# Kernel tuning notes

Measured on AMD Instinct MI355X. Metric: run time of the kernel, lower is better.

## Reference

```python
import jax, jax.numpy as jnp
import numpy as np

CLIP = 5.0  # clip_value from init


def setup_inputs() -> dict:
    key = jax.random.key(0)
    ks = jax.random.split(key, 6)
    B, T, I, H = 128, 1024, 256, 512
    s = 1.0 / np.sqrt(H)
    return {
        "x": jax.random.normal(ks[0], (B, T, I), dtype=jnp.float32),
        "h0": jax.random.normal(ks[1], (1, H), dtype=jnp.float32),
        "w_ih": jax.random.normal(ks[2], (3 * H, I), dtype=jnp.float32) * s,
        "w_hh": jax.random.normal(ks[3], (3 * H, H), dtype=jnp.float32) * s,
        "b_ih": jax.random.normal(ks[4], (3 * H,), dtype=jnp.float32) * s,
        "b_hh": jax.random.normal(ks[5], (3 * H,), dtype=jnp.float32) * s,
    }


def reference(x, h0, w_ih, w_hh, b_ih, b_hh):
    # x: [B, T, I], h0: [1, H]
    B = x.shape[0]
    h_init = jnp.tile(h0, (B, 1))  # [B, H]
    # Precompute all input projections in one big GEMM: [T, B, 3H]
    gi_all = jnp.einsum('bti,gi->tbg', x, w_ih) + b_ih

    def step(h, gi):
        gh = h @ w_hh.T + b_hh                      # [B, 3H]
        ir, iz, inn = jnp.split(gi, 3, axis=-1)
        hr, hz, hn = jnp.split(gh, 3, axis=-1)
        r = jax.nn.sigmoid(ir + hr)
        z = jax.nn.sigmoid(iz + hz)
        n = jnp.tanh(inn + r * hn)
        h_new = (1.0 - z) * n + z * h
        h_new = jnp.clip(h_new, -CLIP, CLIP)
        return h_new, h_new

    h_last, out = jax.lax.scan(step, h_init, gi_all)  # out: [T, B, H]
    output = jnp.transpose(out, (1, 0, 2))            # [B, T, H]
    return output, h_last
```

## Files before the change

### kernel.cpp

```cpp
#include <hip/hip_runtime.h>
#include <math.h>

#define T_SEQ 1024
#define B_SZ  128
#define I_SZ  256
#define H_SZ  512
#define G_SZ  1536

#define NBS   8
#define MB    16
#define NHS   16
#define HB    32
#define GB    96
#define NTHR  384
#define PGB   384

#define SENT32 0x7FFF7FFFu

typedef _Float16 f16;
typedef _Float16 half8 __attribute__((ext_vector_type(8)));
typedef _Float16 f16x4 __attribute__((ext_vector_type(4)));
typedef float f32x4 __attribute__((ext_vector_type(4)));
typedef unsigned uint32x4 __attribute__((ext_vector_type(4)));

__device__ __forceinline__ f32x4 cload_f4(const void* p) {
    f32x4 v;
    asm volatile("global_load_dwordx4 %0, %1, off sc0 sc1" : "=v"(v) : "v"(p));
    return v;
}
__device__ __forceinline__ void cstore_f4(void* p, f32x4 v) {
    asm volatile("global_store_dwordx4 %0, %1, off sc0 sc1" :: "v"(p), "v"(v) : "memory");
}
__device__ __forceinline__ void cstore_u32(void* p, unsigned v) {
    asm volatile("global_store_dword %0, %1, off sc0 sc1" :: "v"(p), "v"(v) : "memory");
}
__device__ __forceinline__ f16x4 load_f16x4_nw(const void* p) {
    f16x4 v;
    asm volatile("global_load_dwordx2 %0, %1, off" : "=v"(v) : "v"(p));
    return v;
}
__device__ __forceinline__ void wait_vm0() {
    asm volatile("s_waitcnt vmcnt(0)" ::: "memory");
    __builtin_amdgcn_sched_barrier(0);
}
__device__ __forceinline__ bool stale4(f32x4 v) {
    uint32x4 u = __builtin_bit_cast(uint32x4, v);
    return (u[0] == SENT32) | (u[1] == SENT32) | (u[2] == SENT32) | (u[3] == SENT32);
}

__global__ void setup_kernel(const float* __restrict__ w_ih,
                             const float* __restrict__ w_hh,
                             const float* __restrict__ h0,
                             f16* __restrict__ wp16,
                             f16* __restrict__ wf16,
                             f16* __restrict__ hbuf) {
    const int i0 = blockIdx.x * blockDim.x + threadIdx.x;
    const int stride = gridDim.x * blockDim.x;
    for (int i = i0; i < I_SZ * G_SZ; i += stride)
        wp16[i] = (f16)w_ih[i];
    for (int i = i0; i < NHS * GB * H_SZ; i += stride) {
        int hs  = i / (GB * H_SZ);
        int rem = i % (GB * H_SZ);
        int gl = rem / H_SZ, k = rem % H_SZ;
        int gate = gl >> 5, c = gl & 31;
        int gg = gate * H_SZ + hs * HB + c;
        wf16[i] = (f16)w_hh[(size_t)gg * H_SZ + k];
    }
    const int hph = B_SZ * H_SZ;
    const f16 sent = __builtin_bit_cast(f16, (unsigned short)0x7FFF);
    for (int i = i0; i < 3 * hph; i += stride) {
        if (i < hph) hbuf[i] = (f16)h0[i & (H_SZ - 1)];
        else         hbuf[i] = sent;
    }
}

__global__ __launch_bounds__(512, 1)
void proj_kernel(const float* __restrict__ x,
                 const f16* __restrict__ wp16,
                 const float* __restrict__ b_ih,
                 f16* __restrict__ gi16) {
    const int t  = blockIdx.x >> 2;
    const int g0 = (blockIdx.x & 3) * PGB;
    const int tid  = threadIdx.x;
    const int wid  = tid >> 6;
    const int lane = tid & 63;
    const int col  = lane & 15;
    const int krow = lane >> 4;

    __shared__ __align__(16) unsigned char x_lds[128 * 512];

    #pragma unroll
    for (int j = 0; j < 8; ++j) {
        int idx = tid + j * 512;
        int b = idx >> 5, k16 = idx & 31;
        const float* xp = x + ((size_t)b * T_SEQ + t) * I_SZ + k16 * 8;
        float4 v0 = *reinterpret_cast<const float4*>(xp);
        float4 v1 = *reinterpret_cast<const float4*>(xp + 4);
        half8 hv;
        hv[0] = (f16)v0.x; hv[1] = (f16)v0.y; hv[2] = (f16)v0.z; hv[3] = (f16)v0.w;
        hv[4] = (f16)v1.x; hv[5] = (f16)v1.y; hv[6] = (f16)v1.z; hv[7] = (f16)v1.w;
        unsigned addr = ((unsigned)(b * 512 + k16 * 16)) ^ (((unsigned)(b & 7)) << 4);
        *reinterpret_cast<half8*>(x_lds + addr) = hv;
    }

    const int gw0 = g0 + wid * 48;
    half8 af[3][8];
    #pragma unroll
    for (int m = 0; m < 3; ++m)
        #pragma unroll
        for (int k = 0; k < 8; ++k)
            af[m][k] = *reinterpret_cast<const half8*>(
                wp16 + (size_t)(gw0 + m * 16 + col) * I_SZ + k * 32 + krow * 8);

    float bias[3][4];
    #pragma unroll
    for (int m = 0; m < 3; ++m)
        #pragma unroll
        for (int r = 0; r < 4; ++r)
            bias[m][r] = b_ih[gw0 + m * 16 + krow * 4 + r];

    __syncthreads();

    #pragma unroll
    for (int nt = 0; nt < 8; ++nt) {
        const int b0 = nt * 16;
        f32x4 acc0 = {0.f,0.f,0.f,0.f}, acc1 = {0.f,0.f,0.f,0.f}, acc2 = {0.f,0.f,0.f,0.f};
        const int brow = b0 + col;
        const unsigned bswz = ((unsigned)(brow & 7)) << 4;
        #pragma unroll
        for (int k = 0; k < 8; ++k) {
            half8 bf = *reinterpret_cast<const half8*>(
                x_lds + (((unsigned)(brow * 512 + k * 64 + krow * 16)) ^ bswz));
            acc0 = __builtin_amdgcn_mfma_f32_16x16x32_f16(af[0][k], bf, acc0, 0, 0, 0);
            acc1 = __builtin_amdgcn_mfma_f32_16x16x32_f16(af[1][k], bf, acc1, 0, 0, 0);
            acc2 = __builtin_amdgcn_mfma_f32_16x16x32_f16(af[2][k], bf, acc2, 0, 0, 0);
        }
        const int pbs = brow >> 4;
        const int pm  = brow & 15;
        #pragma unroll
        for (int r = 0; r < 4; ++r) {
            int gr = gw0 + krow * 4 + r;
            gi16[((size_t)(t * NBS + pbs) * G_SZ + gr)      * MB + pm] = (f16)(acc0[r] + bias[0][r]);
            gi16[((size_t)(t * NBS + pbs) * G_SZ + gr + 16) * MB + pm] = (f16)(acc1[r] + bias[1][r]);
            gi16[((size_t)(t * NBS + pbs) * G_SZ + gr + 32) * MB + pm] = (f16)(acc2[r] + bias[2][r]);
        }
    }
}

__global__ __launch_bounds__(NTHR, 1)
void gru_persist(const f16* __restrict__ gi,
                 const f16* __restrict__ wf16,
                 const float* __restrict__ h0,
                 const float* __restrict__ b_hh,
                 f16* __restrict__ hbuf,
                 float* __restrict__ out) {
    const int bs  = blockIdx.x & (NBS - 1);
    const int hs  = blockIdx.x >> 3;
    const int tid = threadIdx.x;

    __shared__ __align__(16) unsigned char h_lds[MB * H_SZ * 2];
    __shared__ float act_r[MB][HB + 1];
    __shared__ float act_z[MB][HB + 1];
    __shared__ float act_n[MB][HB + 1];
    __shared__ float act_i[MB][HB + 1];

    const int wid  = tid >> 6;
    const int lane = tid & 63;
    const int gate = wid >> 1;
    const int sub  = wid & 1;
    const int col  = lane & 15;
    const int krow = lane >> 4;
    const int c_local = sub * 16 + col;
    const int g_glob  = gate * H_SZ + hs * HB + c_local;

    half8 bfrag[16];
    {
        const f16* wp = wf16 + ((size_t)hs * GB + gate * HB + c_local) * H_SZ
                             + krow * 8;
        #pragma unroll
        for (int kk = 0; kk < 16; ++kk)
            bfrag[kk] = *reinterpret_cast<const half8*>(wp + kk * 32);
    }
    const float bias = b_hh[g_glob];

    const int cb = tid >> 4;
    const int cc = (tid & 15) * 2;
    float hm0 = 0.f, hm1 = 0.f;
    if (tid < 256) { hm0 = h0[hs * HB + cc]; hm1 = h0[hs * HB + cc + 1]; }

    const unsigned a_base = (unsigned)(col * 1024 + krow * 16);
    const unsigned a_swz  = ((unsigned)(col & 7)) << 4;

    const int i0 = tid, i1 = tid + NTHR, i2 = tid + 2 * NTHR;
    const bool has2 = (i2 < 1024);
    const f32x4 sentv = __builtin_bit_cast(f32x4,
        (uint32x4){SENT32, SENT32, SENT32, SENT32});

    const size_t phase_sz = (size_t)B_SZ * H_SZ;

    for (int t = 0; t < T_SEQ; ++t) {
        const int pc = t % 3;
        const int pn = (t + 1) % 3;
        const int pa = (t + 2) % 3;
        const f16* hin = hbuf + (size_t)pc * phase_sz;
        f16* hnx = hbuf + (size_t)pn * phase_sz;
        f16* harm = hbuf + (size_t)pa * phase_sz;

        f16x4 gv = load_f16x4_nw(
            gi + ((size_t)(t * NBS + bs) * G_SZ + g_glob) * MB + krow * 4);

        const f16* a0p = hin + (size_t)(bs * MB + (i0 >> 6)) * H_SZ + (i0 & 63) * 8;
        const f16* a1p = hin + (size_t)(bs * MB + (i1 >> 6)) * H_SZ + (i1 & 63) * 8;
        const f16* a2p = hin + (size_t)(bs * MB + (i2 >> 6)) * H_SZ + (i2 & 63) * 8;
        f32x4 v0 = cload_f4(a0p);
        f32x4 v1 = cload_f4(a1p);
        f32x4 v2;
        if (has2) v2 = cload_f4(a2p);
        wait_vm0();
        {
            int guard = 0;
            bool s0 = stale4(v0), s1 = stale4(v1), s2 = has2 && stale4(v2);
            while (__any(s0 | s1 | s2)) {
                if (s0) v0 = cload_f4((const void*)a0p);
                if (s1) v1 = cload_f4((const void*)a1p);
                if (s2) v2 = cload_f4((const void*)a2p);
                wait_vm0();
                s0 = stale4(v0); s1 = stale4(v1); s2 = has2 && stale4(v2);
                if (++guard > (1 << 20)) break;
            }
        }

        {
            unsigned l0 = ((unsigned)((i0 >> 6) * 1024 + (i0 & 63) * 16))
                          ^ (((unsigned)((i0 >> 6) & 7)) << 4);
            *reinterpret_cast<f32x4*>(h_lds + l0) = v0;
            unsigned l1 = ((unsigned)((i1 >> 6) * 1024 + (i1 & 63) * 16))
                          ^ (((unsigned)((i1 >> 6) & 7)) << 4);
            *reinterpret_cast<f32x4*>(h_lds + l1) = v1;
            if (has2) {
                unsigned l2 = ((unsigned)((i2 >> 6) * 1024 + (i2 & 63) * 16))
                              ^ (((unsigned)((i2 >> 6) & 7)) << 4);
                *reinterpret_cast<f32x4*>(h_lds + l2) = v2;
            }
            if (tid < 64) {
                int row = tid >> 2, g = tid & 3;
                cstore_f4(harm + (size_t)(bs * MB + row) * H_SZ + hs * HB + g * 8,
                          sentv);
            }
        }
        __syncthreads();

        f32x4 acc = {0.f, 0.f, 0.f, 0.f};
        #pragma unroll
        for (int kk = 0; kk < 16; ++kk) {
            half8 av = *reinterpret_cast<const half8*>(
                h_lds + ((a_base + kk * 64) ^ a_swz));
            acc = __builtin_amdgcn_mfma_f32_16x16x32_f16(av, bfrag[kk], acc, 0, 0, 0);
        }
        wait_vm0();

        if (gate == 0) {
            #pragma unroll
            for (int r = 0; r < 4; ++r)
                act_r[krow * 4 + r][c_local] =
                    1.f / (1.f + __expf(-(acc[r] + bias + (float)gv[r])));
        } else if (gate == 1) {
            #pragma unroll
            for (int r = 0; r < 4; ++r)
                act_z[krow * 4 + r][c_local] =
                    1.f / (1.f + __expf(-(acc[r] + bias + (float)gv[r])));
        } else {
            #pragma unroll
            for (int r = 0; r < 4; ++r) {
                act_n[krow * 4 + r][c_local] = acc[r] + bias;
                act_i[krow * 4 + r][c_local] = (float)gv[r];
            }
        }
        __syncthreads();

        if (tid < 256) {
            float r0 = act_r[cb][cc],     r1 = act_r[cb][cc + 1];
            float z0 = act_z[cb][cc],     z1 = act_z[cb][cc + 1];
            float a0 = act_i[cb][cc]     + r0 * act_n[cb][cc];
            float a1 = act_i[cb][cc + 1] + r1 * act_n[cb][cc + 1];
            float n0 = 1.f - 2.f / (__expf(2.f * a0) + 1.f);
            float n1 = 1.f - 2.f / (__expf(2.f * a1) + 1.f);
            float hn0 = (1.f - z0) * n0 + z0 * hm0;
            float hn1 = (1.f - z1) * n1 + z1 * hm1;
            hn0 = fminf(fmaxf(hn0, -5.f), 5.f);
            hn1 = fminf(fmaxf(hn1, -5.f), 5.f);
            hm0 = hn0; hm1 = hn1;

            const int bg = bs * MB + cb;
            const int hg = hs * HB + cc;

            f16 p0 = (f16)hn0, p1 = (f16)hn1;
            unsigned pack = (unsigned)__builtin_bit_cast(unsigned short, p0)
                          | ((unsigned)__builtin_bit_cast(unsigned short, p1) << 16);
            cstore_u32(hnx + (size_t)bg * H_SZ + hg, pack);

            *reinterpret_cast<float2*>(
                out + ((size_t)bg * T_SEQ + t) * H_SZ + hg) = make_float2(hn0, hn1);

            if (t == T_SEQ - 1)
                *reinterpret_cast<float2*>(
                    out + (size_t)B_SZ * T_SEQ * H_SZ + (size_t)bg * H_SZ + hg) =
                    make_float2(hn0, hn1);
        }
    }
}

extern "C" void kernel_launch(void* const* d_in, const int* in_sizes, int n_in,
                              void* d_out, int out_size, void* d_ws, size_t ws_size,
                              hipStream_t stream) {
    const float* x    = (const float*)d_in[0];
    const float* h0   = (const float*)d_in[1];
    const float* w_ih = (const float*)d_in[2];
    const float* w_hh = (const float*)d_in[3];
    const float* b_ih = (const float*)d_in[4];
    const float* b_hh = (const float*)d_in[5];
    float* out = (float*)d_out;

    char* p = (char*)d_ws;
    f16* wp16 = (f16*)p;   p += (size_t)I_SZ * G_SZ * 2;
    f16* wf16 = (f16*)p;   p += (size_t)NHS * GB * H_SZ * 2;
    f16* hbuf = (f16*)p;   p += (size_t)3 * B_SZ * H_SZ * 2;
    f16* gi   = (f16*)p;

    setup_kernel<<<512, 256, 0, stream>>>(w_ih, w_hh, h0, wp16, wf16, hbuf);

    proj_kernel<<<T_SEQ * 4, 512, 0, stream>>>(x, wp16, b_ih, gi);

    gru_persist<<<NBS * NHS, NTHR, 0, stream>>>(gi, wf16, h0, b_hh, hbuf, out);
}
```

Measured before the change: 3.353 ms.

## Halve persistent GRU grid; each block handles two batch slices with 64-wide hidden tiles

The persistent recurrent kernel now runs 32 blocks instead of 128. Each block owns 64 hidden columns (192 gate rows) and serially processes two batch slices per timestep. Half the recurrent weights stay in registers and the other half live in LDS. The h-state buffers become per-batch-slice triple buffers, and the update step writes 4 elements per thread. The intent is to cut the number of blocks in the cross-block spin-wait handshake and the global h traffic per step. The cost is twice the MFMA and LDS work per block, two serialized chains per step, and a heavier LDS footprint.

Measured after the change: 4.899 ms. 1.46x slower.

```diff
diff --git a/kernel.cpp b/kernel.cpp
--- a/kernel.cpp
+++ b/kernel.cpp
@@ -8,12 +8,15 @@
 #define G_SZ  1536
 
 #define NBS   8
+#define NPC   4
 #define MB    16
-#define NHS   16
-#define HB    32
-#define GB    96
+#define NHS   8
+#define HB    64
+#define GB    192
 #define NTHR  384
 #define PGB   384
+#define PH    (MB * H_SZ)
+#define SLC   (3 * PH)
 
 #define SENT32 0x7FFF7FFFu
 
@@ -21,6 +24,7 @@
 typedef _Float16 half8 __attribute__((ext_vector_type(8)));
 typedef _Float16 f16x4 __attribute__((ext_vector_type(4)));
 typedef float f32x4 __attribute__((ext_vector_type(4)));
+typedef unsigned uint32x2 __attribute__((ext_vector_type(2)));
 typedef unsigned uint32x4 __attribute__((ext_vector_type(4)));
 
 __device__ __forceinline__ f32x4 cload_f4(const void* p) {
@@ -31,8 +35,8 @@
 __device__ __forceinline__ void cstore_f4(void* p, f32x4 v) {
     asm volatile("global_store_dwordx4 %0, %1, off sc0 sc1" :: "v"(p), "v"(v) : "memory");
 }
-__device__ __forceinline__ void cstore_u32(void* p, unsigned v) {
-    asm volatile("global_store_dword %0, %1, off sc0 sc1" :: "v"(p), "v"(v) : "memory");
+__device__ __forceinline__ void cstore_u2(void* p, uint32x2 v) {
+    asm volatile("global_store_dwordx2 %0, %1, off sc0 sc1" :: "v"(p), "v"(v) : "memory");
 }
 __device__ __forceinline__ f16x4 load_f16x4_nw(const void* p) {
     f16x4 v;
@@ -62,15 +66,16 @@
         int hs  = i / (GB * H_SZ);
         int rem = i % (GB * H_SZ);
         int gl = rem / H_SZ, k = rem % H_SZ;
-        int gate = gl >> 5, c = gl & 31;
+        int gate = gl >> 6, c = gl & 63;
         int gg = gate * H_SZ + hs * HB + c;
         wf16[i] = (f16)w_hh[(size_t)gg * H_SZ + k];
     }
-    const int hph = B_SZ * H_SZ;
+    const int htot = NBS * SLC;
     const f16 sent = __builtin_bit_cast(f16, (unsigned short)0x7FFF);
-    for (int i = i0; i < 3 * hph; i += stride) {
-        if (i < hph) hbuf[i] = (f16)h0[i & (H_SZ - 1)];
-        else         hbuf[i] = sent;
+    for (int i = i0; i < htot; i += stride) {
+        int j = i % SLC;
+        int phase = j / PH;
+        hbuf[i] = (phase == 0) ? (f16)h0[j & (H_SZ - 1)] : sent;
     }
 }
 
@@ -154,10 +159,13 @@
                  const float* __restrict__ b_hh,
                  f16* __restrict__ hbuf,
                  float* __restrict__ out) {
-    const int bs  = blockIdx.x & (NBS - 1);
-    const int hs  = blockIdx.x >> 3;
-    const int tid = threadIdx.x;
-
+    const int pcid = blockIdx.x & (NPC - 1);
+    const int hs   = blockIdx.x >> 2;
+    const int bsA  = pcid * 2;
+    const int bsB  = pcid * 2 + 1;
+    const int tid  = threadIdx.x;
+
+    __shared__ __align__(16) unsigned char w_lds[96 * 1024];
     __shared__ __align__(16) unsigned char h_lds[MB * H_SZ * 2];
     __shared__ float act_r[MB][HB + 1];
     __shared__ float act_z[MB][HB + 1];
@@ -166,147 +174,179 @@
 
     const int wid  = tid >> 6;
     const int lane = tid & 63;
-    const int gate = wid >> 1;
-    const int sub  = wid & 1;
     const int col  = lane & 15;
     const int krow = lane >> 4;
-    const int c_local = sub * 16 + col;
-    const int g_glob  = gate * H_SZ + hs * HB + c_local;
-
+
+    const int ttR = wid, ttL = wid + 6;
+    const int gateR = ttR >> 2, gateL = ttL >> 2;
+    const int gcR = (ttR & 3) * 16 + col;
+    const int gcL = (ttL & 3) * 16 + col;
+    const int ggR = gateR * H_SZ + hs * HB + gcR;
+    const int ggL = gateL * H_SZ + hs * HB + gcL;
+    const float biasR = b_hh[ggR];
+    const float biasL = b_hh[ggL];
+
+    const f16* wbase = wf16 + (size_t)hs * GB * H_SZ;
+
+    for (int i = tid; i < 96 * 64; i += NTHR) {
+        int r = i >> 6, k8 = i & 63;
+        f32x4 v = *reinterpret_cast<const f32x4*>(
+            wbase + (size_t)(96 + r) * H_SZ + k8 * 8);
+        unsigned addr = ((unsigned)(r * 1024 + k8 * 16)) ^ (((unsigned)(r & 7)) << 4);
+        *reinterpret_cast<f32x4*>(w_lds + addr) = v;
+    }
     half8 bfrag[16];
     {
-        const f16* wp = wf16 + ((size_t)hs * GB + gate * HB + c_local) * H_SZ
-                             + krow * 8;
+        const f16* wp = wbase + (size_t)(ttR * 16 + col) * H_SZ + krow * 8;
         #pragma unroll
         for (int kk = 0; kk < 16; ++kk)
             bfrag[kk] = *reinterpret_cast<const half8*>(wp + kk * 32);
     }
-    const float bias = b_hh[g_glob];
-
-    const int cb = tid >> 4;
-    const int cc = (tid & 15) * 2;
-    float hm0 = 0.f, hm1 = 0.f;
-    if (tid < 256) { hm0 = h0[hs * HB + cc]; hm1 = h0[hs * HB + cc + 1]; }
+
+    const int cb  = tid >> 4;
+    const int cc4 = (tid & 15) * 4;
+    f32x4 hmA = {0.f,0.f,0.f,0.f}, hmB = {0.f,0.f,0.f,0.f};
+    if (tid < 256) {
+        #pragma unroll
+        for (int u = 0; u < 4; ++u) { hmA[u] = h0[hs * HB + cc4 + u]; hmB[u] = hmA[u]; }
+    }
 
     const unsigned a_base = (unsigned)(col * 1024 + krow * 16);
     const unsigned a_swz  = ((unsigned)(col & 7)) << 4;
+    const unsigned b_base = (unsigned)((wid * 16 + col) * 1024 + krow * 16);
 
     const int i0 = tid, i1 = tid + NTHR, i2 = tid + 2 * NTHR;
-    const bool has2 = (i2 < 1024);
+    const bool has2 = (tid < 256);
     const f32x4 sentv = __builtin_bit_cast(f32x4,
         (uint32x4){SENT32, SENT32, SENT32, SENT32});
 
-    const size_t phase_sz = (size_t)B_SZ * H_SZ;
+    f16* hbA = hbuf + (size_t)bsA * SLC;
+    f16* hbB = hbuf + (size_t)bsB * SLC;
+
+    __syncthreads();
 
     for (int t = 0; t < T_SEQ; ++t) {
-        const int pc = t % 3;
-        const int pn = (t + 1) % 3;
-        const int pa = (t + 2) % 3;
-        const f16* hin = hbuf + (size_t)pc * phase_sz;
-        f16* hnx = hbuf + (size_t)pn * phase_sz;
-        f16* harm = hbuf + (size_t)pa * phase_sz;
-
-        f16x4 gv = load_f16x4_nw(
-            gi + ((size_t)(t * NBS + bs) * G_SZ + g_glob) * MB + krow * 4);
-
-        const f16* a0p = hin + (size_t)(bs * MB + (i0 >> 6)) * H_SZ + (i0 & 63) * 8;
-        const f16* a1p = hin + (size_t)(bs * MB + (i1 >> 6)) * H_SZ + (i1 & 63) * 8;
-        const f16* a2p = hin + (size_t)(bs * MB + (i2 >> 6)) * H_SZ + (i2 & 63) * 8;
-        f32x4 v0 = cload_f4(a0p);
-        f32x4 v1 = cload_f4(a1p);
-        f32x4 v2;
-        if (has2) v2 = cload_f4(a2p);
-        wait_vm0();
-        {
-            int guard = 0;
-            bool s0 = stale4(v0), s1 = stale4(v1), s2 = has2 && stale4(v2);
-            while (__any(s0 | s1 | s2)) {
-                if (s0) v0 = cload_f4((const void*)a0p);
-                if (s1) v1 = cload_f4((const void*)a1p);
-                if (s2) v2 = cload_f4((const void*)a2p);
-                wait_vm0();
-                s0 = stale4(v0); s1 = stale4(v1); s2 = has2 && stale4(v2);
-                if (++guard > (1 << 20)) break;
-            }
-        }
-
-        {
-            unsigned l0 = ((unsigned)((i0 >> 6) * 1024 + (i0 & 63) * 16))
-                          ^ (((unsigned)((i0 >> 6) & 7)) << 4);
-            *reinterpret_cast<f32x4*>(h_lds + l0) = v0;
-            unsigned l1 = ((unsigned)((i1 >> 6) * 1024 + (i1 & 63) * 16))
-                          ^ (((unsigned)((i1 >> 6) & 7)) << 4);
-            *reinterpret_cast<f32x4*>(h_lds + l1) = v1;
-            if (has2) {
-                unsigned l2 = ((unsigned)((i2 >> 6) * 1024 + (i2 & 63) * 16))
-                              ^ (((unsigned)((i2 >> 6) & 7)) << 4);
-                *reinterpret_cast<f32x4*>(h_lds + l2) = v2;
-            }
-            if (tid < 64) {
-                int row = tid >> 2, g = tid & 3;
-                cstore_f4(harm + (size_t)(bs * MB + row) * H_SZ + hs * HB + g * 8,
-                          sentv);
-            }
-        }
-        __syncthreads();
-
-        f32x4 acc = {0.f, 0.f, 0.f, 0.f};
-        #pragma unroll
-        for (int kk = 0; kk < 16; ++kk) {
-            half8 av = *reinterpret_cast<const half8*>(
-                h_lds + ((a_base + kk * 64) ^ a_swz));
-            acc = __builtin_amdgcn_mfma_f32_16x16x32_f16(av, bfrag[kk], acc, 0, 0, 0);
-        }
-        wait_vm0();
-
-        if (gate == 0) {
+        const size_t pcO = (size_t)(t % 3) * PH;
+        const size_t pnO = (size_t)((t + 1) % 3) * PH;
+        const size_t paO = (size_t)((t + 2) % 3) * PH;
+
+        auto chain = [&](f16* hb, int bs, f32x4& hm) {
+            f16x4 gvR = load_f16x4_nw(
+                gi + ((size_t)(t * NBS + bs) * G_SZ + ggR) * MB + krow * 4);
+            f16x4 gvL = load_f16x4_nw(
+                gi + ((size_t)(t * NBS + bs) * G_SZ + ggL) * MB + krow * 4);
+
+            const f16* hin = hb + pcO;
+            const f16* a0p = hin + (i0 >> 6) * H_SZ + (i0 & 63) * 8;
+            const f16* a1p = hin + (i1 >> 6) * H_SZ + (i1 & 63) * 8;
+            const f16* a2p = hin + (i2 >> 6) * H_SZ + (i2 & 63) * 8;
+            f32x4 v0 = cload_f4(a0p);
+            f32x4 v1 = cload_f4(a1p);
+            f32x4 v2;
+            if (has2) v2 = cload_f4(a2p);
+            wait_vm0();
+            {
+                int guard = 0;
+                bool s0 = stale4(v0), s1 = stale4(v1), s2 = has2 && stale4(v2);
+                while (__any(s0 | s1 | s2)) {
+                    if (s0) v0 = cload_f4((const void*)a0p);
+                    if (s1) v1 = cload_f4((const void*)a1p);
+                    if (s2) v2 = cload_f4((const void*)a2p);
+                    wait_vm0();
+                    s0 = stale4(v0); s1 = stale4(v1); s2 = has2 && stale4(v2);
+                    if (++guard > (1 << 20)) break;
+                }
+            }
+
+            {
+                unsigned l0 = ((unsigned)((i0 >> 6) * 1024 + (i0 & 63) * 16))
+                              ^ (((unsigned)((i0 >> 6) & 7)) << 4);
+                *reinterpret_cast<f32x4*>(h_lds + l0) = v0;
+                unsigned l1 = ((unsigned)((i1 >> 6) * 1024 + (i1 & 63) * 16))
+                              ^ (((unsigned)((i1 >> 6) & 7)) << 4);
+                *reinterpret_cast<f32x4*>(h_lds + l1) = v1;
+                if (has2) {
+                    unsigned l2 = ((unsigned)((i2 >> 6) * 1024 + (i2 & 63) * 16))
+                                  ^ (((unsigned)((i2 >> 6) & 7)) << 4);
+                    *reinterpret_cast<f32x4*>(h_lds + l2) = v2;
+                }
+                if (tid < 128) {
+                    int row = tid >> 3, g = tid & 7;
+                    cstore_f4(hb + paO + (size_t)row * H_SZ + hs * HB + g * 8,
+                              sentv);
+                }
+            }
+            __syncthreads();
+
+            f32x4 accR = {0.f,0.f,0.f,0.f}, accL = {0.f,0.f,0.f,0.f};
             #pragma unroll
-            for (int r = 0; r < 4; ++r)
-                act_r[krow * 4 + r][c_local] =
-                    1.f / (1.f + __expf(-(acc[r] + bias + (float)gv[r])));
-        } else if (gate == 1) {
-            #pragma unroll
-            for (int r = 0; r < 4; ++r)
-                act_z[krow * 4 + r][c_local] =
-                    1.f / (1.f + __expf(-(acc[r] + bias + (float)gv[r])));
-        } else {
-            #pragma unroll
-            for (int r = 0; r < 4; ++r) {
-                act_n[krow * 4 + r][c_local] = acc[r] + bias;
-                act_i[krow * 4 + r][c_local] = (float)gv[r];
-            }
-        }
-        __syncthreads();
-
-        if (tid < 256) {
-            float r0 = act_r[cb][cc],     r1 = act_r[cb][cc + 1];
-            float z0 = act_z[cb][cc],     z1 = act_z[cb][cc + 1];
-            float a0 = act_i[cb][cc]     + r0 * act_n[cb][cc];
-            float a1 = act_i[cb][cc + 1] + r1 * act_n[cb][cc + 1];
-            float n0 = 1.f - 2.f / (__expf(2.f * a0) + 1.f);
-            float n1 = 1.f - 2.f / (__expf(2.f * a1) + 1.f);
-            float hn0 = (1.f - z0) * n0 + z0 * hm0;
-            float hn1 = (1.f - z1) * n1 + z1 * hm1;
-            hn0 = fminf(fmaxf(hn0, -5.f), 5.f);
-            hn1 = fminf(fmaxf(hn1, -5.f), 5.f);
-            hm0 = hn0; hm1 = hn1;
-
-            const int bg = bs * MB + cb;
-            const int hg = hs * HB + cc;
-
-            f16 p0 = (f16)hn0, p1 = (f16)hn1;
-            unsigned pack = (unsigned)__builtin_bit_cast(unsigned short, p0)
-                          | ((unsigned)__builtin_bit_cast(unsigned short, p1) << 16);
-            cstore_u32(hnx + (size_t)bg * H_SZ + hg, pack);
-
-            *reinterpret_cast<float2*>(
-                out + ((size_t)bg * T_SEQ + t) * H_SZ + hg) = make_float2(hn0, hn1);
-
-            if (t == T_SEQ - 1)
-                *reinterpret_cast<float2*>(
-                    out + (size_t)B_SZ * T_SEQ * H_SZ + (size_t)bg * H_SZ + hg) =
-                    make_float2(hn0, hn1);
-        }
+            for (int kk = 0; kk < 16; ++kk) {
+                half8 av = *reinterpret_cast<const half8*>(
+                    h_lds + ((a_base + kk * 64) ^ a_swz));
+                half8 bv = *reinterpret_cast<const half8*>(
+                    w_lds + ((b_base + kk * 64) ^ a_swz));
+                accR = __builtin_amdgcn_mfma_f32_16x16x32_f16(av, bfrag[kk], accR, 0, 0, 0);
+                accL = __builtin_amdgcn_mfma_f32_16x16x32_f16(av, bv,        accL, 0, 0, 0);
+            }
+            wait_vm0();
+
+            if (gateR == 0) {
+                #pragma unroll
+                for (int r = 0; r < 4; ++r)
+                    act_r[krow * 4 + r][gcR] = accR[r] + biasR + (float)gvR[r];
+            } else {
+                #pragma unroll
+                for (int r = 0; r < 4; ++r)
+                    act_z[krow * 4 + r][gcR] = accR[r] + biasR + (float)gvR[r];
+            }
+            if (gateL == 1) {
+                #pragma unroll
+                for (int r = 0; r < 4; ++r)
+                    act_z[krow * 4 + r][gcL] = accL[r] + biasL + (float)gvL[r];
+            } else {
+                #pragma unroll
+                for (int r = 0; r < 4; ++r) {
+                    act_n[krow * 4 + r][gcL] = accL[r] + biasL;
+                    act_i[krow * 4 + r][gcL] = (float)gvL[r];
+                }
+            }
+            __syncthreads();
+
+            if (tid < 256) {
+                float h4[4];
+                unsigned short us[4];
+                #pragma unroll
+                for (int u = 0; u < 4; ++u) {
+                    int c = cc4 + u;
+                    float r = 1.f / (1.f + __expf(-act_r[cb][c]));
+                    float z = 1.f / (1.f + __expf(-act_z[cb][c]));
+                    float a = act_i[cb][c] + r * act_n[cb][c];
+                    float n = 1.f - 2.f / (__expf(2.f * a) + 1.f);
+                    float hn = (1.f - z) * n + z * hm[u];
+                    hn = fminf(fmaxf(hn, -5.f), 5.f);
+                    hm[u] = hn;
+                    h4[u] = hn;
+                    us[u] = __builtin_bit_cast(unsigned short, (f16)hn);
+                }
+                uint32x2 pk;
+                pk[0] = (unsigned)us[0] | ((unsigned)us[1] << 16);
+                pk[1] = (unsigned)us[2] | ((unsigned)us[3] << 16);
+                const int hg = hs * HB + cc4;
+                cstore_u2(hb + pnO + (size_t)cb * H_SZ + hg, pk);
+
+                const int bg = bs * MB + cb;
+                *reinterpret_cast<float4*>(
+                    out + ((size_t)bg * T_SEQ + t) * H_SZ + hg) =
+                    make_float4(h4[0], h4[1], h4[2], h4[3]);
+                if (t == T_SEQ - 1)
+                    *reinterpret_cast<float4*>(
+                        out + (size_t)B_SZ * T_SEQ * H_SZ + (size_t)bg * H_SZ + hg) =
+                        make_float4(h4[0], h4[1], h4[2], h4[3]);
+            }
+        };
+
+        chain(hbA, bsA, hmA);
+        chain(hbB, bsB, hmB);
     }
 }
 
@@ -324,12 +364,12 @@
     char* p = (char*)d_ws;
     f16* wp16 = (f16*)p;   p += (size_t)I_SZ * G_SZ * 2;
     f16* wf16 = (f16*)p;   p += (size_t)NHS * GB * H_SZ * 2;
-    f16* hbuf = (f16*)p;   p += (size_t)3 * B_SZ * H_SZ * 2;
+    f16* hbuf = (f16*)p;   p += (size_t)NBS * SLC * 2;
     f16* gi   = (f16*)p;
 
     setup_kernel<<<512, 256, 0, stream>>>(w_ih, w_hh, h0, wp16, wf16, hbuf);
 
     proj_kernel<<<T_SEQ * 4, 512, 0, stream>>>(x, wp16, b_ih, gi);
 
-    gru_persist<<<NBS * NHS, NTHR, 0, stream>>>(gi, wf16, h0, b_hh, hbuf, out);
-}
+    gru_persist<<<NPC * NHS, NTHR, 0, stream>>>(gi, wf16, h0, b_hh, hbuf, out);
+}
```
